# Optimization experiments

Measured on AMD Instinct MI355X. Metric: run time of the kernel, lower is better.

Reference implementation:

```python
import jax, jax.numpy as jnp
import numpy as np

N = 200000
E = 6400000
G = 2048
HID = 32
EPS = 1e-5


def setup_inputs() -> dict:
    key = jax.random.key(0)
    ks = jax.random.split(key, 12)
    x = jax.random.normal(ks[0], (N, 1), dtype=jnp.float32)
    edge_index = jax.random.randint(ks[1], (2, E), 0, N, dtype=jnp.int64)
    batch = jnp.sort(jax.random.randint(ks[2], (N,), 0, G, dtype=jnp.int64))
    s1 = 1.0  # fan_in=1
    s2 = 1.0 / np.sqrt(HID)
    return {
        "x": x,
        "edge_index": edge_index,
        "batch": batch,
        # SAGEConv1: lin_l (neighbors, with bias) and lin_r (root, no bias)
        "W1l": jax.random.normal(ks[3], (HID, 1), jnp.float32) * s1,
        "b1l": jnp.zeros((HID,), jnp.float32),
        "W1r": jax.random.normal(ks[4], (HID, 1), jnp.float32) * s1,
        # SAGEConv2
        "W2l": jax.random.normal(ks[5], (HID, HID), jnp.float32) * s2,
        "b2l": jnp.zeros((HID,), jnp.float32),
        "W2r": jax.random.normal(ks[6], (HID, HID), jnp.float32) * s2,
        # BatchNorms (affine)
        "g1": jnp.ones((HID,), jnp.float32),
        "be1": jnp.zeros((HID,), jnp.float32),
        "g2": jnp.ones((HID,), jnp.float32),
        "be2": jnp.zeros((HID,), jnp.float32),
        # attention gate Linear(hidden, 1)
        "gate_w": jax.random.normal(ks[7], (1, HID), jnp.float32) * s2,
        "gate_b": jnp.zeros((1,), jnp.float32),
        # final Linear(hidden, 1)
        "lin_w": jax.random.normal(ks[8], (1, HID), jnp.float32) * s2,
        "lin_b": jnp.zeros((1,), jnp.float32),
    }


def _sage(x, src, dst, Wl, bl, Wr):
    # mean aggregation of neighbor messages x_j = x[src] at dst
    msg = x[src]                                              # [E, F]
    agg = jax.ops.segment_sum(msg, dst, num_segments=N)       # [N, F]
    deg = jax.ops.segment_sum(jnp.ones((src.shape[0], 1), x.dtype), dst, num_segments=N)
    agg = agg / jnp.maximum(deg, 1.0)
    return agg @ Wl.T + bl + x @ Wr.T


def _bn(x, gamma, beta):
    mu = jnp.mean(x, axis=0)
    var = jnp.mean((x - mu) ** 2, axis=0)  # biased variance, as torch BN
    return (x - mu) * jax.lax.rsqrt(var + EPS) * gamma + beta


def reference(x, edge_index, batch, W1l, b1l, W1r, W2l, b2l, W2r,
              g1, be1, g2, be2, gate_w, gate_b, lin_w, lin_b):
    src, dst = edge_index[0], edge_index[1]
    h = jax.nn.relu(_bn(_sage(x, src, dst, W1l, b1l, W1r), g1, be1))
    h = jax.nn.relu(_bn(_sage(h, src, dst, W2l, b2l, W2r), g2, be2))
    # attentional aggregation: segment softmax over gate scores
    score = (h @ gate_w.T + gate_b)                           # [N, 1]
    smax = jax.ops.segment_max(score, batch, num_segments=G)  # [G, 1]
    ex = jnp.exp(score - smax[batch])
    denom = jax.ops.segment_sum(ex, batch, num_segments=G)    # [G, 1]
    alpha = ex / denom[batch]
    g = jax.ops.segment_sum(alpha * h, batch, num_segments=G) # [G, HID]
    return jax.nn.sigmoid((g @ lin_w.T + lin_b)[:, 0])
```

## Files before the change

kernel.cpp:

```cpp
#include <hip/hip_runtime.h>
#include <math.h>

#define N_NODES 200000
#define N_EDGES 6400000
#define N_GRAPHS 2048
#define HID 32
#define BN_EPS 1e-5f

#define NPB 256
#define NBUCK ((N_NODES + NPB - 1) / NPB)
#define CAP 8960
#define PART_CHUNK 8192
#define NPARTBLK ((N_EDGES + PART_CHUNK - 1) / PART_CHUNK)

#define NPC 64
#define NBLK_C (N_NODES / NPC)

#define RED_BLKS 64
#define RED_CHUNK ((NBLK_C + RED_BLKS - 1) / RED_BLKS)

__device__ inline float relu_f(float v) { return fmaxf(v, 0.f); }

__global__ void k_init(int* __restrict__ cursor) {
    int t = blockIdx.x * blockDim.x + threadIdx.x;
    if (t < NBUCK) cursor[t] = t * CAP;
}

__launch_bounds__(256)
__global__ void k_part(const int* __restrict__ src, const int* __restrict__ dst,
                       int* __restrict__ cursor, unsigned int* __restrict__ ebuf) {
    __shared__ int histL[NBUCK];
    __shared__ int baseL[NBUCK];
    int tid = threadIdx.x;
    for (int i = tid; i < NBUCK; i += 256) histL[i] = 0;
    __syncthreads();
    int e0 = blockIdx.x * PART_CHUNK;
    int e1 = min(e0 + PART_CHUNK, N_EDGES);
    int4 dreg[8];
    int4 rreg[8];
#pragma unroll
    for (int i = 0; i < 8; i++) {
        int base = e0 + (i * 256 + tid) * 4;
        if (base < e1) {
            int4 d4 = *(const int4*)(dst + base);
            dreg[i] = d4;
            rreg[i].x = atomicAdd(&histL[d4.x >> 8], 1);
            rreg[i].y = atomicAdd(&histL[d4.y >> 8], 1);
            rreg[i].z = atomicAdd(&histL[d4.z >> 8], 1);
            rreg[i].w = atomicAdd(&histL[d4.w >> 8], 1);
        } else {
            dreg[i] = make_int4(-1, -1, -1, -1);
        }
    }
    __syncthreads();
    for (int i = tid; i < NBUCK; i += 256) {
        int c = histL[i];
        if (c) baseL[i] = atomicAdd(&cursor[i], c);
    }
    __syncthreads();
#pragma unroll
    for (int i = 0; i < 8; i++) {
        int base = e0 + (i * 256 + tid) * 4;
        if (base < e1) {
            int4 s4 = *(const int4*)(src + base);
            int4 d4 = dreg[i];
            int4 r4 = rreg[i];
            int b, pos;
            b = d4.x >> 8; pos = baseL[b] + r4.x;
            if (pos < (b + 1) * CAP) ebuf[pos] = (unsigned)(s4.x & 0x3FFFF) | ((unsigned)(d4.x & 255) << 18);
            b = d4.y >> 8; pos = baseL[b] + r4.y;
            if (pos < (b + 1) * CAP) ebuf[pos] = (unsigned)(s4.y & 0x3FFFF) | ((unsigned)(d4.y & 255) << 18);
            b = d4.z >> 8; pos = baseL[b] + r4.z;
            if (pos < (b + 1) * CAP) ebuf[pos] = (unsigned)(s4.z & 0x3FFFF) | ((unsigned)(d4.z & 255) << 18);
            b = d4.w >> 8; pos = baseL[b] + r4.w;
            if (pos < (b + 1) * CAP) ebuf[pos] = (unsigned)(s4.w & 0x3FFFF) | ((unsigned)(d4.w & 255) << 18);
        }
    }
}

__launch_bounds__(256)
__global__ void k_sort(const unsigned int* __restrict__ ebuf, const int* __restrict__ cursor,
                       const float* __restrict__ x, int* __restrict__ ebuf2,
                       int* __restrict__ deg, int* __restrict__ offs,
                       float* __restrict__ ax, float* __restrict__ part1) {
    __shared__ int degL[NPB], scanL[NPB], offL[NPB];
    __shared__ float red[4][5];
    int tid = threadIdx.x;
    degL[tid] = 0;
    __syncthreads();
    int b = blockIdx.x;
    int p0 = b * CAP;
    int cnt = min(cursor[b] - p0, CAP);
    int rk[35];
#pragma unroll
    for (int it = 0; it < 35; it++) {
        int i = tid + it * 256;
        if (i < cnt) rk[it] = atomicAdd(&degL[ebuf[p0 + i] >> 18], 1);
    }
    __syncthreads();
    int d = degL[tid];
    scanL[tid] = d;
    __syncthreads();
    for (int off = 1; off < NPB; off <<= 1) {
        int y = (tid >= off) ? scanL[tid - off] : 0;
        __syncthreads();
        scanL[tid] += y;
        __syncthreads();
    }
    int myoff = scanL[tid] - d;
    offL[tid] = myoff;
    __syncthreads();
    int node = b * NPB + tid;
    if (node < N_NODES) { deg[node] = d; offs[node] = p0 + myoff; }
#pragma unroll
    for (int it = 0; it < 35; it++) {
        int i = tid + it * 256;
        if (i < cnt) {
            unsigned v = ebuf[p0 + i];
            int ld = v >> 18;
            ebuf2[p0 + offL[ld] + rk[it]] = (int)(v & 0x3FFFF);
        }
    }
    __syncthreads();
    float sum = 0.f;
    int base = p0 + myoff;
    int j = 0;
    for (; j + 8 <= d; j += 8) {
        int ss[8];
#pragma unroll
        for (int k = 0; k < 8; k++) ss[k] = ebuf2[base + j + k];
        float acc = 0.f;
#pragma unroll
        for (int k = 0; k < 8; k++) acc += x[ss[k]];
        sum += acc;
    }
    for (; j < d; j++) sum += x[ebuf2[base + j]];
    float an = 0.f, xn = 0.f;
    if (node < N_NODES) {
        an = sum / (float)max(d, 1);
        xn = x[node];
        ax[2 * node] = an;
        ax[2 * node + 1] = xn;
    }
    float sa = an, sx = xn, saa = an * an, sxx = xn * xn, sax = an * xn;
    for (int o = 32; o; o >>= 1) {
        sa += __shfl_down(sa, o);
        sx += __shfl_down(sx, o);
        saa += __shfl_down(saa, o);
        sxx += __shfl_down(sxx, o);
        sax += __shfl_down(sax, o);
    }
    int w = tid >> 6;
    if ((tid & 63) == 0) {
        red[w][0] = sa; red[w][1] = sx; red[w][2] = saa; red[w][3] = sxx; red[w][4] = sax;
    }
    __syncthreads();
    if (tid < 5)
        part1[b * 8 + tid] = red[0][tid] + red[1][tid] + red[2][tid] + red[3][tid];
}

__launch_bounds__(256)
__global__ void k_params1(const float* __restrict__ part1,
                          const float* __restrict__ W1l, const float* __restrict__ b1l,
                          const float* __restrict__ W1r, const float* __restrict__ g1,
                          const float* __restrict__ be1, float* __restrict__ pABC) {
    int tid = threadIdx.x;
    double loc[5] = {0, 0, 0, 0, 0};
    for (int b = tid; b < NBUCK; b += 256) {
#pragma unroll
        for (int s = 0; s < 5; s++) loc[s] += (double)part1[b * 8 + s];
    }
    for (int o = 32; o; o >>= 1) {
#pragma unroll
        for (int s = 0; s < 5; s++) loc[s] += __shfl_down(loc[s], o);
    }
    __shared__ double red[4][5];
    __shared__ double st[5];
    int w = tid >> 6;
    if ((tid & 63) == 0) {
#pragma unroll
        for (int s = 0; s < 5; s++) red[w][s] = loc[s];
    }
    __syncthreads();
    if (tid < 5) st[tid] = red[0][tid] + red[1][tid] + red[2][tid] + red[3][tid];
    __syncthreads();
    int f = tid;
    if (f < HID) {
        double invN = 1.0 / (double)N_NODES;
        double ma = st[0] * invN, mx = st[1] * invN;
        double va = st[2] * invN - ma * ma;
        double vx = st[3] * invN - mx * mx;
        double cax = st[4] * invN - ma * mx;
        double wl = (double)W1l[f], wr = (double)W1r[f];
        double mu = wl * ma + wr * mx + (double)b1l[f];
        double var = wl * wl * va + wr * wr * vx + 2.0 * wl * wr * cax;
        double s = (double)g1[f] / sqrt(var + (double)BN_EPS);
        pABC[f] = (float)(wl * s);
        pABC[HID + f] = (float)(wr * s);
        pABC[2 * HID + f] = (float)(((double)b1l[f] - mu) * s + (double)be1[f]);
    }
}

__launch_bounds__(256)
__global__ void k_conv2(const int* __restrict__ ebuf2, const int* __restrict__ offs,
                        const int* __restrict__ deg, const float* __restrict__ ax,
                        const float* __restrict__ pABC,
                        const float* __restrict__ W2l, const float* __restrict__ W2r,
                        const float* __restrict__ b2l, float* __restrict__ h2pre,
                        float* __restrict__ part2) {
    __shared__ float aggL[NPC * (HID + 1)];
    __shared__ __align__(16) float2 pairL[8 * 32];
    __shared__ float A_s[HID], B_s[HID], C_s[HID];
    __shared__ int degS[NPC], offS[NPC];
    int tid = threadIdx.x;
    int b = blockIdx.x;
    if (tid < HID) {
        A_s[tid] = pABC[tid];
        B_s[tid] = pABC[HID + tid];
        C_s[tid] = pABC[2 * HID + tid];
    }
    if (tid < NPC) {
        degS[tid] = deg[b * NPC + tid];
        offS[tid] = offs[b * NPC + tid];
    }
    __syncthreads();
    int f = tid & 31;
    int grp = tid >> 5;
    float Af = A_s[f], Bf = B_s[f], Cf = C_s[f];
    const float2* ax2 = (const float2*)ax;
    float2* myStage = pairL + grp * 32;
    const float4* myStage4 = (const float4*)myStage;
    float m = 0.f;
    int iC = 0, jC = 0;
    float2 pvP = make_float2(0.f, 0.f);
    {
        int rem0 = min(32, degS[grp]);
        if (f < rem0) pvP = ax2[ebuf2[offS[grp] + f]];
    }
#pragma unroll 1
    while (iC < 8) {
        int dgC = degS[iC * 8 + grp];
        int iN = iC, jN = jC + 32;
        if (jN >= dgC) { iN = iC + 1; jN = 0; }
        float2 pvN = make_float2(0.f, 0.f);
        if (iN < 8) {
            int slotN = iN * 8 + grp;
            int remN = min(32, degS[slotN] - jN);
            if (f < remN) pvN = ax2[ebuf2[offS[slotN] + jN + f]];
        }
        int rem = min(32, dgC - jC);
        myStage[f] = pvP;
        int k = 0;
        for (; k + 2 <= rem; k += 2) {
            float4 q = myStage4[k >> 1];
            m += relu_f(fmaf(q.x, Af, fmaf(q.y, Bf, Cf)));
            m += relu_f(fmaf(q.z, Af, fmaf(q.w, Bf, Cf)));
        }
        if (k < rem) {
            float2 q = myStage[k];
            m += relu_f(fmaf(q.x, Af, fmaf(q.y, Bf, Cf)));
        }
        if (iN != iC) {
            int ln = iC * 8 + grp;
            aggL[ln * (HID + 1) + f] = m / (float)max(dgC, 1);
            m = 0.f;
        }
        iC = iN; jC = jN;
        pvP = pvN;
    }
    __syncthreads();
    int nl = tid & 63;
    int fg = tid >> 6;
    int node = b * NPC + nl;
    float2 axn = ax2[node];
    float an = axn.x, xn = axn.y;
    float ag[HID], h1[HID];
#pragma unroll
    for (int k = 0; k < HID; k++) {
        ag[k] = aggL[nl * (HID + 1) + k];
        h1[k] = relu_f(fmaf(an, A_s[k], fmaf(xn, B_s[k], C_s[k])));
    }
    float v[8];
#pragma unroll
    for (int lf = 0; lf < 8; lf++) {
        int ff = fg * 8 + lf;
        const float4* wl4 = (const float4*)(W2l + ff * HID);
        const float4* wr4 = (const float4*)(W2r + ff * HID);
        float s = b2l[ff];
#pragma unroll
        for (int q = 0; q < HID / 4; q++) {
            float4 wl = wl4[q], wr = wr4[q];
            s = fmaf(ag[4 * q],     wl.x, fmaf(h1[4 * q],     wr.x, s));
            s = fmaf(ag[4 * q + 1], wl.y, fmaf(h1[4 * q + 1], wr.y, s));
            s = fmaf(ag[4 * q + 2], wl.z, fmaf(h1[4 * q + 2], wr.z, s));
            s = fmaf(ag[4 * q + 3], wl.w, fmaf(h1[4 * q + 3], wr.w, s));
        }
        v[lf] = s;
    }
    float4* op = (float4*)(h2pre + (size_t)node * HID + fg * 8);
    op[0] = make_float4(v[0], v[1], v[2], v[3]);
    op[1] = make_float4(v[4], v[5], v[6], v[7]);
#pragma unroll
    for (int lf = 0; lf < 8; lf++) {
        float s1v = v[lf], s2v = v[lf] * v[lf];
        for (int o = 32; o; o >>= 1) {
            s1v += __shfl_down(s1v, o);
            s2v += __shfl_down(s2v, o);
        }
        if (nl == 0) {
            part2[(size_t)b * 64 + fg * 8 + lf] = s1v;
            part2[(size_t)b * 64 + 32 + fg * 8 + lf] = s2v;
        }
    }
}

__launch_bounds__(256)
__global__ void k_red2(const float* __restrict__ part2, double* __restrict__ mid) {
    __shared__ double st2[4][64];
    int tid = threadIdx.x;
    int q = tid >> 6, t = tid & 63;
    int b0 = blockIdx.x * RED_CHUNK;
    int b1 = min(b0 + RED_CHUNK, NBLK_C);
    double s = 0.0;
    for (int b = b0 + q; b < b1; b += 4) s += (double)part2[(size_t)b * 64 + t];
    st2[q][t] = s;
    __syncthreads();
    if (tid < 64)
        mid[(size_t)blockIdx.x * 64 + tid] = st2[0][tid] + st2[1][tid] + st2[2][tid] + st2[3][tid];
}

__launch_bounds__(256)
__global__ void k_params2(const double* __restrict__ mid, const float* __restrict__ g2,
                          const float* __restrict__ be2, float* __restrict__ pPQ) {
    __shared__ double st2[4][64];
    __shared__ double st[64];
    int tid = threadIdx.x;
    int q = tid >> 6, t = tid & 63;
    double s = 0.0;
    for (int i = q; i < RED_BLKS; i += 4) s += mid[(size_t)i * 64 + t];
    st2[q][t] = s;
    __syncthreads();
    if (tid < 64) st[tid] = st2[0][tid] + st2[1][tid] + st2[2][tid] + st2[3][tid];
    __syncthreads();
    if (tid < HID) {
        double invN = 1.0 / (double)N_NODES;
        double mu = st[tid] * invN;
        double var = st[HID + tid] * invN - mu * mu;
        double sc = (double)g2[tid] / sqrt(var + (double)BN_EPS);
        pPQ[tid] = (float)sc;
        pPQ[HID + tid] = (float)((double)be2[tid] - mu * sc);
    }
}

#define FIN_TPB 128
__launch_bounds__(FIN_TPB)
__global__ void k_final(const float* __restrict__ h2pre, const int* __restrict__ batch,
                        const float* __restrict__ pPQ, const float* __restrict__ gate_w,
                        const float* __restrict__ gate_b, const float* __restrict__ lin_w,
                        const float* __restrict__ lin_b, float* __restrict__ out) {
    __shared__ int sh_lo, sh_hi;
    __shared__ float red[2][HID + 2];
    __shared__ float sh_P[HID], sh_Q[HID], sh_gw[HID], sh_lw[HID];
    int g = blockIdx.x;
    if (threadIdx.x == 0) {
        int lo = 0, hi = N_NODES;
        while (lo < hi) { int mid = (lo + hi) >> 1; if (batch[mid] < g) lo = mid + 1; else hi = mid; }
        sh_lo = lo;
        int lo2 = lo, hi2 = N_NODES;
        int key2 = g + 1;
        while (lo2 < hi2) { int mid = (lo2 + hi2) >> 1; if (batch[mid] < key2) lo2 = mid + 1; else hi2 = mid; }
        sh_hi = lo2;
    }
    if (threadIdx.x < HID) {
        sh_P[threadIdx.x] = pPQ[threadIdx.x];
        sh_Q[threadIdx.x] = pPQ[HID + threadIdx.x];
        sh_gw[threadIdx.x] = gate_w[threadIdx.x];
        sh_lw[threadIdx.x] = lin_w[threadIdx.x];
    }
    __syncthreads();
    int lo = sh_lo, hi = sh_hi;
    float gb = gate_b[0];

    float mx = -3.0e38f;
    for (int n = lo + threadIdx.x; n < hi; n += FIN_TPB) {
        const float4* hp = (const float4*)(h2pre + (size_t)n * HID);
        float sc = gb;
#pragma unroll
        for (int i = 0; i < HID / 4; i++) {
            float4 v = hp[i];
            sc += relu_f(fmaf(v.x, sh_P[4 * i], sh_Q[4 * i])) * sh_gw[4 * i];
            sc += relu_f(fmaf(v.y, sh_P[4 * i + 1], sh_Q[4 * i + 1])) * sh_gw[4 * i + 1];
            sc += relu_f(fmaf(v.z, sh_P[4 * i + 2], sh_Q[4 * i + 2])) * sh_gw[4 * i + 2];
            sc += relu_f(fmaf(v.w, sh_P[4 * i + 3], sh_Q[4 * i + 3])) * sh_gw[4 * i + 3];
        }
        mx = fmaxf(mx, sc);
    }
    for (int o = 32; o; o >>= 1) mx = fmaxf(mx, __shfl_down(mx, o));
    if ((threadIdx.x & 63) == 0) red[threadIdx.x >> 6][0] = mx;
    __syncthreads();
    float smax = fmaxf(red[0][0], red[1][0]);
    __syncthreads();

    float S = 0.f;
    float T[HID];
#pragma unroll
    for (int f = 0; f < HID; f++) T[f] = 0.f;
    for (int n = lo + threadIdx.x; n < hi; n += FIN_TPB) {
        const float4* hp = (const float4*)(h2pre + (size_t)n * HID);
        float h[HID];
        float sc = gb;
#pragma unroll
        for (int i = 0; i < HID / 4; i++) {
            float4 v = hp[i];
            h[4 * i]     = relu_f(fmaf(v.x, sh_P[4 * i],     sh_Q[4 * i]));
            h[4 * i + 1] = relu_f(fmaf(v.y, sh_P[4 * i + 1], sh_Q[4 * i + 1]));
            h[4 * i + 2] = relu_f(fmaf(v.z, sh_P[4 * i + 2], sh_Q[4 * i + 2]));
            h[4 * i + 3] = relu_f(fmaf(v.w, sh_P[4 * i + 3], sh_Q[4 * i + 3]));
            sc += h[4 * i] * sh_gw[4 * i] + h[4 * i + 1] * sh_gw[4 * i + 1]
                + h[4 * i + 2] * sh_gw[4 * i + 2] + h[4 * i + 3] * sh_gw[4 * i + 3];
        }
        float e = __expf(sc - smax);
        S += e;
#pragma unroll
        for (int f = 0; f < HID; f++) T[f] += e * h[f];
    }
    for (int o = 32; o; o >>= 1) {
        S += __shfl_down(S, o);
#pragma unroll
        for (int f = 0; f < HID; f++) T[f] += __shfl_down(T[f], o);
    }
    if ((threadIdx.x & 63) == 0) {
        int w = threadIdx.x >> 6;
        red[w][1] = S;
#pragma unroll
        for (int f = 0; f < HID; f++) red[w][2 + f] = T[f];
    }
    __syncthreads();
    if (threadIdx.x == 0) {
        float St = red[0][1] + red[1][1];
        float z = lin_b[0];
        if (St > 0.f) {
            float inv = 1.f / St;
#pragma unroll
            for (int f = 0; f < HID; f++)
                z += (red[0][2 + f] + red[1][2 + f]) * inv * sh_lw[f];
        }
        out[g] = 1.f / (1.f + __expf(-z));
    }
}

extern "C" void kernel_launch(void* const* d_in, const int* in_sizes, int n_in,
                              void* d_out, int out_size, void* d_ws, size_t ws_size,
                              hipStream_t stream) {
    const float* x = (const float*)d_in[0];
    const int* ei = (const int*)d_in[1];
    const int* batch = (const int*)d_in[2];
    const float* W1l = (const float*)d_in[3];
    const float* b1l = (const float*)d_in[4];
    const float* W1r = (const float*)d_in[5];
    const float* W2l = (const float*)d_in[6];
    const float* b2l = (const float*)d_in[7];
    const float* W2r = (const float*)d_in[8];
    const float* g1 = (const float*)d_in[9];
    const float* be1 = (const float*)d_in[10];
    const float* g2 = (const float*)d_in[11];
    const float* be2 = (const float*)d_in[12];
    const float* gate_w = (const float*)d_in[13];
    const float* gate_b = (const float*)d_in[14];
    const float* lin_w = (const float*)d_in[15];
    const float* lin_b = (const float*)d_in[16];

    const int* srcp = ei;
    const int* dstp = ei + N_EDGES;

    char* ws = (char*)d_ws;
    size_t p = 0;
    auto alloc = [&](size_t bytes) -> char* {
        char* r = ws + p;
        p = (p + bytes + 255) & ~(size_t)255;
        return r;
    };
    unsigned int* ebuf = (unsigned int*)alloc((size_t)NBUCK * CAP * 4);
    int* ebuf2 = (int*)alloc((size_t)NBUCK * CAP * 4);
    float* ax = (float*)alloc((size_t)N_NODES * 2 * 4);
    int* deg = (int*)alloc((size_t)N_NODES * 4);
    int* offs = (int*)alloc((size_t)N_NODES * 4);
    int* cursor = (int*)alloc((size_t)NBUCK * 4);
    float* pABC = (float*)alloc(96 * 4);
    float* pPQ = (float*)alloc(64 * 4);
    float* part1 = (float*)alloc((size_t)NBUCK * 8 * 4);
    float* part2 = (float*)alloc((size_t)NBLK_C * 64 * 4);
    double* mid = (double*)alloc((size_t)RED_BLKS * 64 * 8);
    float* h2pre = (float*)ebuf;

    k_init<<<1, 1024, 0, stream>>>(cursor);
    k_part<<<NPARTBLK, 256, 0, stream>>>(srcp, dstp, cursor, ebuf);
    k_sort<<<NBUCK, 256, 0, stream>>>(ebuf, cursor, x, ebuf2, deg, offs, ax, part1);
    k_params1<<<1, 256, 0, stream>>>(part1, W1l, b1l, W1r, g1, be1, pABC);
    k_conv2<<<NBLK_C, 256, 0, stream>>>(ebuf2, offs, deg, ax, pABC, W2l, W2r, b2l, h2pre, part2);
    k_red2<<<RED_BLKS, 256, 0, stream>>>(part2, mid);
    k_params2<<<1, 256, 0, stream>>>(mid, g2, be2, pPQ);
    k_final<<<N_GRAPHS, FIN_TPB, 0, stream>>>(h2pre, batch, pPQ, gate_w, gate_b, lin_w, lin_b,
                                              (float*)d_out);
}
```

Before: 513.9 us.

## Simplify conv2 gather loop and restructure dense stage for lower register use

Replaces the software-pipelined flat gather loop in k_conv2 with a simple nested per-node loop that no longer prefetches the next chunk. The dense 32x32 stage now walks the input in float4 chunks and reads aggregates with vector LDS loads from a 36-wide padded row, instead of holding 64 floats of ag/h1 in registers. Launch bounds request 8 blocks per multiprocessor to raise occupancy. In exchange, the gather loses its explicit prefetch of the next chunk's loads, so memory latency hiding now relies on the extra occupancy.

```diff
diff --git a/kernel.cpp b/kernel.cpp
--- a/kernel.cpp
+++ b/kernel.cpp
@@ -15,6 +15,7 @@
 
 #define NPC 64
 #define NBLK_C (N_NODES / NPC)
+#define AGS 36
 
 #define RED_BLKS 64
 #define RED_CHUNK ((NBLK_C + RED_BLKS - 1) / RED_BLKS)
@@ -201,14 +202,14 @@
     }
 }
 
-__launch_bounds__(256)
+__launch_bounds__(256, 8)
 __global__ void k_conv2(const int* __restrict__ ebuf2, const int* __restrict__ offs,
                         const int* __restrict__ deg, const float* __restrict__ ax,
                         const float* __restrict__ pABC,
                         const float* __restrict__ W2l, const float* __restrict__ W2r,
                         const float* __restrict__ b2l, float* __restrict__ h2pre,
                         float* __restrict__ part2) {
-    __shared__ float aggL[NPC * (HID + 1)];
+    __shared__ __align__(16) float aggL[NPC * AGS];
     __shared__ __align__(16) float2 pairL[8 * 32];
     __shared__ float A_s[HID], B_s[HID], C_s[HID];
     __shared__ int degS[NPC], offS[NPC];
@@ -230,43 +231,29 @@
     const float2* ax2 = (const float2*)ax;
     float2* myStage = pairL + grp * 32;
     const float4* myStage4 = (const float4*)myStage;
-    float m = 0.f;
-    int iC = 0, jC = 0;
-    float2 pvP = make_float2(0.f, 0.f);
-    {
-        int rem0 = min(32, degS[grp]);
-        if (f < rem0) pvP = ax2[ebuf2[offS[grp] + f]];
-    }
 #pragma unroll 1
-    while (iC < 8) {
-        int dgC = degS[iC * 8 + grp];
-        int iN = iC, jN = jC + 32;
-        if (jN >= dgC) { iN = iC + 1; jN = 0; }
-        float2 pvN = make_float2(0.f, 0.f);
-        if (iN < 8) {
-            int slotN = iN * 8 + grp;
-            int remN = min(32, degS[slotN] - jN);
-            if (f < remN) pvN = ax2[ebuf2[offS[slotN] + jN + f]];
-        }
-        int rem = min(32, dgC - jC);
-        myStage[f] = pvP;
-        int k = 0;
-        for (; k + 2 <= rem; k += 2) {
-            float4 q = myStage4[k >> 1];
-            m += relu_f(fmaf(q.x, Af, fmaf(q.y, Bf, Cf)));
-            m += relu_f(fmaf(q.z, Af, fmaf(q.w, Bf, Cf)));
-        }
-        if (k < rem) {
-            float2 q = myStage[k];
-            m += relu_f(fmaf(q.x, Af, fmaf(q.y, Bf, Cf)));
-        }
-        if (iN != iC) {
-            int ln = iC * 8 + grp;
-            aggL[ln * (HID + 1) + f] = m / (float)max(dgC, 1);
-            m = 0.f;
-        }
-        iC = iN; jC = jN;
-        pvP = pvN;
+    for (int i = 0; i < NPC / 8; i++) {
+        int ln = i * 8 + grp;
+        int dg = degS[ln], off = offS[ln];
+        float m = 0.f;
+#pragma unroll 1
+        for (int j = 0; j < dg; j += 32) {
+            int rem = min(32, dg - j);
+            float2 pv = make_float2(0.f, 0.f);
+            if (f < rem) pv = ax2[ebuf2[off + j + f]];
+            myStage[f] = pv;
+            int k = 0;
+            for (; k + 2 <= rem; k += 2) {
+                float4 q = myStage4[k >> 1];
+                m += relu_f(fmaf(q.x, Af, fmaf(q.y, Bf, Cf)));
+                m += relu_f(fmaf(q.z, Af, fmaf(q.w, Bf, Cf)));
+            }
+            if (k < rem) {
+                float2 q = myStage[k];
+                m += relu_f(fmaf(q.x, Af, fmaf(q.y, Bf, Cf)));
+            }
+        }
+        aggL[ln * AGS + f] = m / (float)max(dg, 1);
     }
     __syncthreads();
     int nl = tid & 63;
@@ -274,28 +261,29 @@
     int node = b * NPC + nl;
     float2 axn = ax2[node];
     float an = axn.x, xn = axn.y;
-    float ag[HID], h1[HID];
-#pragma unroll
-    for (int k = 0; k < HID; k++) {
-        ag[k] = aggL[nl * (HID + 1) + k];
-        h1[k] = relu_f(fmaf(an, A_s[k], fmaf(xn, B_s[k], C_s[k])));
-    }
     float v[8];
 #pragma unroll
-    for (int lf = 0; lf < 8; lf++) {
-        int ff = fg * 8 + lf;
-        const float4* wl4 = (const float4*)(W2l + ff * HID);
-        const float4* wr4 = (const float4*)(W2r + ff * HID);
-        float s = b2l[ff];
-#pragma unroll
-        for (int q = 0; q < HID / 4; q++) {
-            float4 wl = wl4[q], wr = wr4[q];
-            s = fmaf(ag[4 * q],     wl.x, fmaf(h1[4 * q],     wr.x, s));
-            s = fmaf(ag[4 * q + 1], wl.y, fmaf(h1[4 * q + 1], wr.y, s));
-            s = fmaf(ag[4 * q + 2], wl.z, fmaf(h1[4 * q + 2], wr.z, s));
-            s = fmaf(ag[4 * q + 3], wl.w, fmaf(h1[4 * q + 3], wr.w, s));
-        }
-        v[lf] = s;
+    for (int lf = 0; lf < 8; lf++) v[lf] = b2l[fg * 8 + lf];
+#pragma unroll
+    for (int q = 0; q < HID / 4; q++) {
+        float4 ag4 = *(const float4*)&aggL[nl * AGS + 4 * q];
+        float4 h14;
+        h14.x = relu_f(fmaf(an, A_s[4 * q],     fmaf(xn, B_s[4 * q],     C_s[4 * q])));
+        h14.y = relu_f(fmaf(an, A_s[4 * q + 1], fmaf(xn, B_s[4 * q + 1], C_s[4 * q + 1])));
+        h14.z = relu_f(fmaf(an, A_s[4 * q + 2], fmaf(xn, B_s[4 * q + 2], C_s[4 * q + 2])));
+        h14.w = relu_f(fmaf(an, A_s[4 * q + 3], fmaf(xn, B_s[4 * q + 3], C_s[4 * q + 3])));
+#pragma unroll
+        for (int lf = 0; lf < 8; lf++) {
+            int ff = fg * 8 + lf;
+            float4 wl = *(const float4*)(W2l + ff * HID + 4 * q);
+            float4 wr = *(const float4*)(W2r + ff * HID + 4 * q);
+            float s = v[lf];
+            s = fmaf(ag4.x, wl.x, fmaf(h14.x, wr.x, s));
+            s = fmaf(ag4.y, wl.y, fmaf(h14.y, wr.y, s));
+            s = fmaf(ag4.z, wl.z, fmaf(h14.z, wr.z, s));
+            s = fmaf(ag4.w, wl.w, fmaf(h14.w, wr.w, s));
+            v[lf] = s;
+        }
     }
     float4* op = (float4*)(h2pre + (size_t)node * HID + fg * 8);
     op[0] = make_float4(v[0], v[1], v[2], v[3]);
```

After: 576.7 us. 12.2% more time.

## Process two nodes per warp pass with fully unrolled staging and padding correction

Applied to the files above, without the earlier changes.

The neighbour-aggregation loop in conv2 is restructured so each warp handles two nodes at once, issuing both gathers per round before the reduction. The old variable-length tail is replaced by a fixed 16-step unrolled loop over the 32-entry stage. Padded zero entries contribute relu(C) each, and that amount is subtracted afterwards. This aims to raise memory-level parallelism and drop the branchy per-chunk bookkeeping. In exchange it does wasted work when the two degrees differ and when degrees are not multiples of 32, and it drops the explicit next-chunk prefetch.

```diff
diff --git a/kernel.cpp b/kernel.cpp
--- a/kernel.cpp
+++ b/kernel.cpp
@@ -209,7 +209,7 @@
                         const float* __restrict__ b2l, float* __restrict__ h2pre,
                         float* __restrict__ part2) {
     __shared__ float aggL[NPC * (HID + 1)];
-    __shared__ __align__(16) float2 pairL[8 * 32];
+    __shared__ __align__(16) float2 stageL[8][2][32];
     __shared__ float A_s[HID], B_s[HID], C_s[HID];
     __shared__ int degS[NPC], offS[NPC];
     int tid = threadIdx.x;
@@ -227,46 +227,42 @@
     int f = tid & 31;
     int grp = tid >> 5;
     float Af = A_s[f], Bf = B_s[f], Cf = C_s[f];
+    float reluC = fmaxf(Cf, 0.f);
     const float2* ax2 = (const float2*)ax;
-    float2* myStage = pairL + grp * 32;
-    const float4* myStage4 = (const float4*)myStage;
-    float m = 0.f;
-    int iC = 0, jC = 0;
-    float2 pvP = make_float2(0.f, 0.f);
-    {
-        int rem0 = min(32, degS[grp]);
-        if (f < rem0) pvP = ax2[ebuf2[offS[grp] + f]];
-    }
+    float2* stA = stageL[grp][0];
+    float2* stB = stageL[grp][1];
+    const float4* stA4 = (const float4*)stA;
+    const float4* stB4 = (const float4*)stB;
 #pragma unroll 1
-    while (iC < 8) {
-        int dgC = degS[iC * 8 + grp];
-        int iN = iC, jN = jC + 32;
-        if (jN >= dgC) { iN = iC + 1; jN = 0; }
-        float2 pvN = make_float2(0.f, 0.f);
-        if (iN < 8) {
-            int slotN = iN * 8 + grp;
-            int remN = min(32, degS[slotN] - jN);
-            if (f < remN) pvN = ax2[ebuf2[offS[slotN] + jN + f]];
-        }
-        int rem = min(32, dgC - jC);
-        myStage[f] = pvP;
-        int k = 0;
-        for (; k + 2 <= rem; k += 2) {
-            float4 q = myStage4[k >> 1];
-            m += relu_f(fmaf(q.x, Af, fmaf(q.y, Bf, Cf)));
-            m += relu_f(fmaf(q.z, Af, fmaf(q.w, Bf, Cf)));
-        }
-        if (k < rem) {
-            float2 q = myStage[k];
-            m += relu_f(fmaf(q.x, Af, fmaf(q.y, Bf, Cf)));
-        }
-        if (iN != iC) {
-            int ln = iC * 8 + grp;
-            aggL[ln * (HID + 1) + f] = m / (float)max(dgC, 1);
-            m = 0.f;
-        }
-        iC = iN; jC = jN;
-        pvP = pvN;
+    for (int p = 0; p < 4; p++) {
+        int lnA = (2 * p) * 8 + grp;
+        int lnB = (2 * p + 1) * 8 + grp;
+        int dgA = degS[lnA], offA = offS[lnA];
+        int dgB = degS[lnB], offB = offS[lnB];
+        int rounds = (max(dgA, dgB) + 31) >> 5;
+        float mA = 0.f, mB = 0.f;
+#pragma unroll 1
+        for (int r = 0; r < rounds; r++) {
+            int j = r * 32;
+            float2 pa = make_float2(0.f, 0.f), pb = make_float2(0.f, 0.f);
+            if (f < dgA - j) pa = ax2[ebuf2[offA + j + f]];
+            if (f < dgB - j) pb = ax2[ebuf2[offB + j + f]];
+            stA[f] = pa;
+            stB[f] = pb;
+#pragma unroll
+            for (int u = 0; u < 16; u++) {
+                float4 qa = stA4[u];
+                mA += relu_f(fmaf(qa.x, Af, fmaf(qa.y, Bf, Cf)));
+                mA += relu_f(fmaf(qa.z, Af, fmaf(qa.w, Bf, Cf)));
+                float4 qb = stB4[u];
+                mB += relu_f(fmaf(qb.x, Af, fmaf(qb.y, Bf, Cf)));
+                mB += relu_f(fmaf(qb.z, Af, fmaf(qb.w, Bf, Cf)));
+            }
+        }
+        mA -= (float)(rounds * 32 - dgA) * reluC;
+        mB -= (float)(rounds * 32 - dgB) * reluC;
+        aggL[lnA * (HID + 1) + f] = mA / (float)max(dgA, 1);
+        aggL[lnB * (HID + 1) + f] = mB / (float)max(dgB, 1);
     }
     __syncthreads();
     int nl = tid & 63;
```

New measurement: 482.2 us. -6.2%, faster.
